# Kernel tuning notes

Measured on AMD Instinct MI355X. Metric: run time of the kernel, lower is better.

Reference implementation:

```python
import math
import jax, jax.numpy as jnp
import numpy as np

T, B, E, H = 1024, 4, 1024, 16
DH = E // H
NUM_BUCKETS = 32
MAX_DISTANCE = 128


def setup_inputs() -> dict:
    key = jax.random.key(0)
    ks = jax.random.split(key, 12)
    s = 0.02
    return {
        "query": jax.random.normal(ks[0], (T, B, E), dtype=jnp.float32),
        "q_w": jax.random.normal(ks[1], (E, E), dtype=jnp.float32) * s,
        "q_b": jax.random.normal(ks[2], (E,), dtype=jnp.float32) * s,
        "k_w": jax.random.normal(ks[3], (E, E), dtype=jnp.float32) * s,
        "k_b": jax.random.normal(ks[4], (E,), dtype=jnp.float32) * s,
        "v_w": jax.random.normal(ks[5], (E, E), dtype=jnp.float32) * s,
        "v_b": jax.random.normal(ks[6], (E,), dtype=jnp.float32) * s,
        "out_w": jax.random.normal(ks[7], (E, E), dtype=jnp.float32) * s,
        "out_b": jnp.zeros((E,), dtype=jnp.float32),
        "rel_bias": jax.random.normal(ks[8], (NUM_BUCKETS, H), dtype=jnp.float32) * s,
        "grep_w": jax.random.normal(ks[9], (8, DH), dtype=jnp.float32) * s,
        "grep_b": jax.random.normal(ks[10], (8,), dtype=jnp.float32) * s,
        "grep_a": jnp.ones((1, H, 1, 1), dtype=jnp.float32),
    }


def _relative_position_buckets(qlen, klen):
    # bidirectional T5-style bucketing
    ctx = jnp.arange(qlen, dtype=jnp.int32)[:, None]
    mem = jnp.arange(klen, dtype=jnp.int32)[None, :]
    rp = mem - ctx  # [qlen, klen]
    n = NUM_BUCKETS // 2
    buckets = (rp > 0).astype(jnp.int32) * n
    arp = jnp.abs(rp)
    max_exact = n // 2
    is_small = arp < max_exact
    # guard log(0): values at arp<max_exact are never selected from the large branch
    large = max_exact + (
        jnp.log(jnp.maximum(arp, 1).astype(jnp.float32) / max_exact)
        / math.log(MAX_DISTANCE / max_exact)
        * (n - max_exact)
    ).astype(jnp.int32)
    large = jnp.minimum(large, n - 1)
    return buckets + jnp.where(is_small, arp, large)


def reference(query, q_w, q_b, k_w, k_b, v_w, v_b, out_w, out_b, rel_bias, grep_w, grep_b, grep_a):
    tgt_len, bsz, embed_dim = query.shape
    scaling = DH ** -0.5

    # relative-position bias [H, T, T]
    buckets = _relative_position_buckets(tgt_len, tgt_len)
    pos_bias = rel_bias[buckets]                     # [T, T, H]
    pos_bias = jnp.transpose(pos_bias, (2, 0, 1))    # [H, T, T]

    # GRU-style gate computed from the *unprojected* query, per head
    qh_raw = jnp.transpose(query, (1, 0, 2)).reshape(bsz, tgt_len, H, DH)
    qh_raw = jnp.transpose(qh_raw, (0, 2, 1, 3))     # [B, H, T, DH]
    g = jnp.einsum("bhtd,ed->bhte", qh_raw, grep_w) + grep_b  # [B,H,T,8]
    g = jax.nn.sigmoid(g.reshape(bsz, H, tgt_len, 2, 4).sum(-1))  # [B,H,T,2]
    gate_a, gate_b = g[..., 0:1], g[..., 1:2]        # [B,H,T,1]
    gate_a_1 = gate_a * (gate_b * grep_a - 1.0) + 2.0
    attn_bias = gate_a_1 * pos_bias[None]            # [B, H, T, T]

    # QKV projections (self-attention: k,v from query)
    q = (query @ q_w.T + q_b) * scaling
    k = query @ k_w.T + k_b
    v = query @ v_w.T + v_b
    qh = jnp.transpose(q.reshape(tgt_len, bsz, H, DH), (1, 2, 0, 3))  # [B,H,T,DH]
    kh = jnp.transpose(k.reshape(tgt_len, bsz, H, DH), (1, 2, 0, 3))
    vh = jnp.transpose(v.reshape(tgt_len, bsz, H, DH), (1, 2, 0, 3))

    scores = jnp.einsum("bhtd,bhsd->bhts", qh, kh) + attn_bias
    probs = jax.nn.softmax(scores, axis=-1)
    ctx = jnp.einsum("bhts,bhsd->bhtd", probs, vh)   # [B,H,T,DH]
    ctx = jnp.transpose(ctx, (2, 0, 1, 3)).reshape(tgt_len, bsz, embed_dim)
    out = ctx @ out_w.T + out_b                      # [T, B, E]
    return out
```

## Files before the change

kernel.cpp:

```cpp
#include <hip/hip_runtime.h>
#include <math.h>

#define T_ 1024
#define B_ 4
#define E_ 1024
#define H_ 16
#define DH_ 64

#define LOG2E 1.44269504088896f

typedef __attribute__((ext_vector_type(8))) __bf16 bf16x8;
typedef __attribute__((ext_vector_type(4))) __bf16 bf16x4;
typedef __attribute__((ext_vector_type(4))) float f32x4;

__device__ __forceinline__ __bf16 f2bf(float x){
  union { unsigned short u; __bf16 b; } cv;
  unsigned u32 = __float_as_uint(x);
  cv.u = (unsigned short)((u32 + 0x7fffu + ((u32 >> 16) & 1u)) >> 16);
  return cv.b;
}
__device__ __forceinline__ __bf16 f2bf_fast(float x){
  union { unsigned short u; __bf16 b; } cv;
  cv.u = (unsigned short)((__float_as_uint(x) + 0x8000u) >> 16);
  return cv.b;
}

__device__ __forceinline__ void glds16(const void* g, void* l){
  __builtin_amdgcn_global_load_lds(
      (__attribute__((address_space(1))) void*)(void*)g,
      (__attribute__((address_space(3))) void*)l,
      16, 0, 0);
}

__global__ __launch_bounds__(256) void prep_kernel(
    const float* __restrict__ q_w, const float* __restrict__ k_w,
    const float* __restrict__ v_w, const float* __restrict__ out_w,
    __bf16* __restrict__ wq, __bf16* __restrict__ wk,
    __bf16* __restrict__ wv, __bf16* __restrict__ wo,
    const float* __restrict__ query, const float* __restrict__ gw,
    const float* __restrict__ gb, const float* __restrict__ ga,
    float* __restrict__ gates, __bf16* __restrict__ qbf,
    const float* __restrict__ rel_bias, float* __restrict__ tab)
{
  const int bid = blockIdx.x;
  const int tid = threadIdx.x;
  if (bid < 4096){
    const float* a; __bf16* o;
    switch (bid >> 10){
      case 0: a = q_w;  o = wq; break;
      case 1: a = k_w;  o = wk; break;
      case 2: a = v_w;  o = wv; break;
      default: a = out_w; o = wo; break;
    }
    int i = ((bid & 1023) * 256 + tid) * 4;
    float4 v = *(const float4*)(a + i);
    bf16x4 r;
    r[0] = f2bf(v.x); r[1] = f2bf(v.y); r[2] = f2bf(v.z); r[3] = f2bf(v.w);
    *(bf16x4*)(o + i) = r;
  } else if (bid < 4352){
    int t = (bid - 4096) * 4 + (tid >> 6);
    int bh = tid & 63;
    int h = bh & 15;
    const float* q = query + (size_t)t * E_ * B_ + bh * 64;
    __bf16* qo = qbf + (size_t)t * E_ * B_ + bh * 64;
    float g[8];
    #pragma unroll
    for (int e = 0; e < 8; e++) g[e] = gb[e];
    #pragma unroll
    for (int c = 0; c < 8; c++){
      float4 v0 = *(const float4*)(q + c * 8);
      float4 v1 = *(const float4*)(q + c * 8 + 4);
      bf16x8 o;
      o[0] = f2bf(v0.x); o[1] = f2bf(v0.y); o[2] = f2bf(v0.z); o[3] = f2bf(v0.w);
      o[4] = f2bf(v1.x); o[5] = f2bf(v1.y); o[6] = f2bf(v1.z); o[7] = f2bf(v1.w);
      *(bf16x8*)(qo + c * 8) = o;
      #pragma unroll
      for (int e = 0; e < 8; e++){
        const float* w = gw + e * 64 + c * 8;
        g[e] += v0.x * w[0] + v0.y * w[1] + v0.z * w[2] + v0.w * w[3]
              + v1.x * w[4] + v1.y * w[5] + v1.z * w[6] + v1.w * w[7];
      }
    }
    float a0 = (g[0] + g[1]) + (g[2] + g[3]);
    float a1 = (g[4] + g[5]) + (g[6] + g[7]);
    float sa = 1.f / (1.f + __expf(-a0));
    float sb = 1.f / (1.f + __expf(-a1));
    gates[bh * T_ + t] = (sa * (sb * ga[h] - 1.0f) + 2.0f) * LOG2E;
  } else {
    int tb = bid - 4352;
    int h = tb >> 3;
    int i = (tb & 7) * 256 + tid;
    if (i < 2047){
      int rp = i - 1023;
      int base = rp > 0 ? 16 : 0;
      int arp = rp < 0 ? -rp : rp;
      int off;
      if (arp < 8) off = arp;
      else {
        float val = (logf((float)arp * 0.125f) / 2.772588722239781f) * 8.0f;
        int lg = (int)val;
        off = 8 + (lg > 7 ? 7 : lg);
      }
      tab[h * 2047 + i] = rel_bias[(base + off) * H_ + h];
    }
  }
}

__global__ __launch_bounds__(256, 2) void gemm_qkv(
    const __bf16* __restrict__ A,
    const __bf16* __restrict__ W0, const __bf16* __restrict__ W1, const __bf16* __restrict__ W2,
    const float* __restrict__ b0, const float* __restrict__ b1, const float* __restrict__ b2,
    __bf16* out0, __bf16* out1, __bf16* out2)
{
  __shared__ __bf16 As[2][128 * 64];
  __shared__ __bf16 Bs[2][3][64 * 64];
  const int tid = threadIdx.x;
  const int lane = tid & 63, wid = tid >> 6;
  const int l15 = lane & 15, quad = lane >> 4;
  const int dd = blockIdx.x;
  const int j = dd >> 3;
  const int m0 = ((dd & 7) * 4 + (j & 3)) * 128;
  const int nt = j >> 2;
  const int n0 = nt * 64;

  f32x4 acc[3][2][4];
  #pragma unroll
  for (int z = 0; z < 3; z++)
    #pragma unroll
    for (int i = 0; i < 2; i++)
      #pragma unroll
      for (int jj = 0; jj < 4; jj++){
        acc[z][i][jj][0] = 0.f; acc[z][i][jj][1] = 0.f;
        acc[z][i][jj][2] = 0.f; acc[z][i][jj][3] = 0.f;
      }

  const int grow = lane >> 3;
  const int gcol = (((lane & 7) ^ grow) * 8);
  const int sw = (l15 & 7);

  auto STAGE = [&](int bi, int k0){
    #pragma unroll
    for (int r = 0; r < 4; r++){
      int rb = wid * 32 + r * 8;
      glds16(A + (size_t)(m0 + rb + grow) * E_ + k0 + gcol, &As[bi][rb * 64]);
    }
    #pragma unroll
    for (int r = 0; r < 2; r++){
      int rb = wid * 16 + r * 8;
      glds16(W0 + (size_t)(n0 + rb + grow) * E_ + k0 + gcol, &Bs[bi][0][rb * 64]);
      glds16(W1 + (size_t)(n0 + rb + grow) * E_ + k0 + gcol, &Bs[bi][1][rb * 64]);
      glds16(W2 + (size_t)(n0 + rb + grow) * E_ + k0 + gcol, &Bs[bi][2][rb * 64]);
    }
  };

  auto COMPUTE = [&](int bi){
    #pragma unroll
    for (int kq = 0; kq < 2; kq++){
      const int ce = ((kq * 4 + quad) ^ sw) * 8;
      bf16x8 am[2];
      #pragma unroll
      for (int i = 0; i < 2; i++) am[i] = *(const bf16x8*)&As[bi][(wid * 32 + i * 16 + l15) * 64 + ce];
      #pragma unroll
      for (int z = 0; z < 3; z++){
        bf16x8 bn[4];
        #pragma unroll
        for (int jj = 0; jj < 4; jj++) bn[jj] = *(const bf16x8*)&Bs[bi][z][(jj * 16 + l15) * 64 + ce];
        #pragma unroll
        for (int i = 0; i < 2; i++)
          #pragma unroll
          for (int jj = 0; jj < 4; jj++)
            acc[z][i][jj] = __builtin_amdgcn_mfma_f32_16x16x32_bf16(am[i], bn[jj], acc[z][i][jj], 0, 0, 0);
      }
    }
  };

  STAGE(0, 0);
  __syncthreads();
  for (int kt = 0; kt < 16; kt += 2){
    STAGE(1, (kt + 1) * 64);
    COMPUTE(0);
    __syncthreads();
    if (kt + 2 < 16) STAGE(0, (kt + 2) * 64);
    COMPUTE(1);
    __syncthreads();
  }

  #pragma unroll
  for (int z = 0; z < 2; z++){
    __bf16* outp = z ? out1 : out0;
    const float* bias = z ? b1 : b0;
    const float scale = z ? 1.0f : 0.125f * LOG2E;
    #pragma unroll
    for (int i = 0; i < 2; i++){
      const int row0 = m0 + wid * 32 + i * 16 + quad * 4;
      #pragma unroll
      for (int jj = 0; jj < 4; jj++){
        const int col = n0 + jj * 16 + l15;
        const float bc = bias[col];
        const int d2 = col & 63;
        #pragma unroll
        for (int r = 0; r < 4; r++){
          float v = (acc[z][i][jj][r] + bc) * scale;
          int row = row0 + r;
          int t = row >> 2, bb = row & 3;
          outp[(size_t)((bb * H_ + nt) * T_ + t) * DH_ + d2] = f2bf(v);
        }
      }
    }
  }

  __syncthreads();
  __bf16 (*vbuf)[4][32] = (__bf16 (*)[4][32])&As[0][0];
  #pragma unroll
  for (int i = 0; i < 2; i++){
    const int t_local = wid * 8 + i * 4 + quad;
    #pragma unroll
    for (int jj = 0; jj < 4; jj++){
      const int nl = jj * 16 + l15;
      const float bc = b2[n0 + nl];
      #pragma unroll
      for (int r = 0; r < 4; r++)
        vbuf[nl][r][t_local] = f2bf(acc[2][i][jj][r] + bc);
    }
  }
  __syncthreads();
  {
    const int nl = tid >> 2;
    const int bb = tid & 3;
    __bf16* dst = out2 + (size_t)((bb * H_ + nt) * DH_ + nl) * T_ + (m0 >> 2);
    const __bf16* src = &vbuf[nl][bb][0];
    #pragma unroll
    for (int c = 0; c < 4; c++)
      *(bf16x8*)(dst + c * 8) = *(const bf16x8*)(src + c * 8);
  }
}

__global__ __launch_bounds__(256) void gemm_out(
    const __bf16* __restrict__ A, const __bf16* __restrict__ W,
    const float* __restrict__ bias, float* __restrict__ out)
{
  __shared__ __bf16 As[2][64 * 64];
  __shared__ __bf16 Bs[2][128 * 64];
  const int tid = threadIdx.x;
  const int lane = tid & 63, wid = tid >> 6;
  const int l15 = lane & 15, quad = lane >> 4;
  const int wm = wid >> 1, wn = wid & 1;
  const int dd = blockIdx.x;
  const int j = dd >> 3;
  const int m0 = ((dd & 7) * 8 + (j & 7)) * 64;
  const int n0 = (j >> 3) * 128;

  f32x4 acc[2][4];
  #pragma unroll
  for (int i = 0; i < 2; i++)
    #pragma unroll
    for (int jj = 0; jj < 4; jj++){
      acc[i][jj][0] = 0.f; acc[i][jj][1] = 0.f; acc[i][jj][2] = 0.f; acc[i][jj][3] = 0.f;
    }

  const int grow = lane >> 3;
  const int gcol = (((lane & 7) ^ grow) * 8);
  const int sw = (l15 & 7);

  auto STAGE = [&](int bi, int k0){
    #pragma unroll
    for (int r = 0; r < 2; r++){
      int rbA = wid * 16 + r * 8;
      glds16(A + (size_t)(m0 + rbA + grow) * E_ + k0 + gcol, &As[bi][rbA * 64]);
    }
    #pragma unroll
    for (int r = 0; r < 4; r++){
      int rbB = wid * 32 + r * 8;
      glds16(W + (size_t)(n0 + rbB + grow) * E_ + k0 + gcol, &Bs[bi][rbB * 64]);
    }
  };

  auto COMPUTE = [&](int bi){
    #pragma unroll
    for (int kq = 0; kq < 2; kq++){
      const int ce = ((kq * 4 + quad) ^ sw) * 8;
      bf16x8 am[2], bn[4];
      #pragma unroll
      for (int i = 0; i < 2; i++) am[i] = *(const bf16x8*)&As[bi][(wm * 32 + i * 16 + l15) * 64 + ce];
      #pragma unroll
      for (int jj = 0; jj < 4; jj++) bn[jj] = *(const bf16x8*)&Bs[bi][(wn * 64 + jj * 16 + l15) * 64 + ce];
      #pragma unroll
      for (int i = 0; i < 2; i++)
        #pragma unroll
        for (int jj = 0; jj < 4; jj++)
          acc[i][jj] = __builtin_amdgcn_mfma_f32_16x16x32_bf16(am[i], bn[jj], acc[i][jj], 0, 0, 0);
    }
  };

  STAGE(0, 0);
  __syncthreads();
  for (int kt = 0; kt < 16; kt += 2){
    STAGE(1, (kt + 1) * 64);
    COMPUTE(0);
    __syncthreads();
    if (kt + 2 < 16) STAGE(0, (kt + 2) * 64);
    COMPUTE(1);
    __syncthreads();
  }

  #pragma unroll
  for (int i = 0; i < 2; i++){
    const int row0 = m0 + wm * 32 + i * 16 + quad * 4;
    #pragma unroll
    for (int jj = 0; jj < 4; jj++){
      const int col = n0 + wn * 64 + jj * 16 + l15;
      const float bc = bias[col];
      #pragma unroll
      for (int r = 0; r < 4; r++)
        out[(size_t)(row0 + r) * E_ + col] = acc[i][jj][r] + bc;
    }
  }
}

__global__ __launch_bounds__(256) void attn_kernel(
    const __bf16* __restrict__ qg, const __bf16* __restrict__ kg, const __bf16* __restrict__ vgT,
    const float* __restrict__ gates, const float* __restrict__ tab,
    __bf16* __restrict__ ctx)
{
  const int LDP = 72;
  __shared__ __bf16 Ks[2][64 * 64];
  __shared__ __bf16 Vt[2][64 * 64];
  __shared__ __bf16 Pt[4][2][16 * LDP];
  __shared__ float tabh[2048];

  const int tid = threadIdx.x;
  const int lane = tid & 63, wid = tid >> 6;
  const int l15 = lane & 15, quad = lane >> 4;
  const int dgrid = blockIdx.x;
  const int j = dgrid >> 3;
  const int bh = (dgrid & 7) + 8 * (j & 7);
  const int tq = j >> 3;
  const int b = bh >> 4, h = bh & 15;
  const __bf16* qb = qg + (size_t)bh * T_ * DH_;
  const __bf16* kb = kg + (size_t)bh * T_ * DH_;
  const __bf16* vb = vgT + (size_t)bh * DH_ * T_;

  for (int i = tid; i < 2047; i += 256) tabh[i] = tab[h * 2047 + i];

  const int t0w = tq * 128 + wid * 32;
  bf16x8 bq[2][2];
  float g[2];
  int ibase[2];
  #pragma unroll
  for (int tg = 0; tg < 2; tg++){
    int t_lane = t0w + tg * 16 + l15;
    bq[tg][0] = *(const bf16x8*)(qb + (size_t)t_lane * DH_ + quad * 8);
    bq[tg][1] = *(const bf16x8*)(qb + (size_t)t_lane * DH_ + 32 + quad * 8);
    g[tg] = gates[bh * T_ + t_lane];
    ibase[tg] = 1023 - t_lane;
  }

  const int grow = lane >> 3;
  const int gcol = (((lane & 7) ^ grow) * 8);
  const int swf = (l15 & 7);

  float l_run[2] = {0.f, 0.f};
  f32x4 O[2][4];
  #pragma unroll
  for (int tg = 0; tg < 2; tg++)
    #pragma unroll
    for (int mt = 0; mt < 4; mt++){ O[tg][mt][0]=0.f; O[tg][mt][1]=0.f; O[tg][mt][2]=0.f; O[tg][mt][3]=0.f; }

  #pragma unroll
  for (int r = 0; r < 2; r++){
    int rb = wid * 16 + r * 8;
    glds16(kb + (size_t)(rb + grow) * DH_ + gcol, &Ks[0][rb * 64]);
    glds16(vb + (size_t)(rb + grow) * T_ + gcol, &Vt[0][rb * 64]);
  }
  __syncthreads();

  for (int it = 0; it < 16; it++){
    const int s0 = it * 64;
    const int cur = it & 1;

    if (it < 15){
      const int sn = s0 + 64;
      #pragma unroll
      for (int r = 0; r < 2; r++){
        int rb = wid * 16 + r * 8;
        glds16(kb + (size_t)(sn + rb + grow) * DH_ + gcol, &Ks[cur ^ 1][rb * 64]);
        glds16(vb + (size_t)(rb + grow) * T_ + sn + gcol, &Vt[cur ^ 1][rb * 64]);
      }
    }

    f32x4 S[2][4];
    #pragma unroll
    for (int nt = 0; nt < 4; nt++){
      const int rowb = (nt * 16 + l15) * 64;
      bf16x8 ak0 = *(const bf16x8*)&Ks[cur][rowb + ((quad ^ swf) * 8)];
      bf16x8 ak1 = *(const bf16x8*)&Ks[cur][rowb + (((4 + quad) ^ swf) * 8)];
      #pragma unroll
      for (int tg = 0; tg < 2; tg++){
        f32x4 a; a[0]=0.f; a[1]=0.f; a[2]=0.f; a[3]=0.f;
        a = __builtin_amdgcn_mfma_f32_16x16x32_bf16(ak0, bq[tg][0], a, 0, 0, 0);
        a = __builtin_amdgcn_mfma_f32_16x16x32_bf16(ak1, bq[tg][1], a, 0, 0, 0);
        S[tg][nt] = a;
      }
    }

    const int drel = s0 - t0w;
    if (drel >= 160 || drel <= -192){
      const float sv = (drel > 0) ? tabh[1151] : tabh[895];
      #pragma unroll
      for (int tg = 0; tg < 2; tg++){
        const float cb = g[tg] * sv;
        #pragma unroll
        for (int nt = 0; nt < 4; nt++)
          #pragma unroll
          for (int r = 0; r < 4; r++)
            S[tg][nt][r] = __builtin_amdgcn_exp2f(S[tg][nt][r] + cb);
      }
    } else {
      #pragma unroll
      for (int tg = 0; tg < 2; tg++){
        const int ib = ibase[tg] + s0;
        #pragma unroll
        for (int nt = 0; nt < 4; nt++)
          #pragma unroll
          for (int r = 0; r < 4; r++)
            S[tg][nt][r] = __builtin_amdgcn_exp2f(S[tg][nt][r] + g[tg] * tabh[ib + nt * 16 + quad * 4 + r]);
      }
    }

    #pragma unroll
    for (int tg = 0; tg < 2; tg++){
      __bf16* pw = &Pt[wid][tg][0];
      #pragma unroll
      for (int nt = 0; nt < 4; nt++){
        bf16x4 p;
        p[0] = f2bf_fast(S[tg][nt][0]); p[1] = f2bf_fast(S[tg][nt][1]);
        p[2] = f2bf_fast(S[tg][nt][2]); p[3] = f2bf_fast(S[tg][nt][3]);
        *(bf16x4*)&pw[l15 * LDP + nt * 16 + quad * 4] = p;
      }
      float rs = 0.f;
      #pragma unroll
      for (int nt = 0; nt < 4; nt++) rs += (S[tg][nt][0] + S[tg][nt][1]) + (S[tg][nt][2] + S[tg][nt][3]);
      rs += __shfl_xor(rs, 16, 64);
      rs += __shfl_xor(rs, 32, 64);
      l_run[tg] += rs;
    }

    #pragma unroll
    for (int ks = 0; ks < 2; ks++){
      bf16x8 bp[2];
      #pragma unroll
      for (int tg = 0; tg < 2; tg++)
        bp[tg] = *(const bf16x8*)&Pt[wid][tg][l15 * LDP + ks * 32 + quad * 8];
      #pragma unroll
      for (int mt = 0; mt < 4; mt++){
        const int rowb = (mt * 16 + l15) * 64;
        bf16x8 av = *(const bf16x8*)&Vt[cur][rowb + (((ks * 4 + quad) ^ swf) * 8)];
        #pragma unroll
        for (int tg = 0; tg < 2; tg++)
          O[tg][mt] = __builtin_amdgcn_mfma_f32_16x16x32_bf16(av, bp[tg], O[tg][mt], 0, 0, 0);
      }
    }

    __syncthreads();
  }

  #pragma unroll
  for (int tg = 0; tg < 2; tg++){
    const int t_lane = t0w + tg * 16 + l15;
    const float inv = 1.f / l_run[tg];
    #pragma unroll
    for (int mt = 0; mt < 4; mt++){
      bf16x4 o;
      o[0] = f2bf(O[tg][mt][0] * inv); o[1] = f2bf(O[tg][mt][1] * inv);
      o[2] = f2bf(O[tg][mt][2] * inv); o[3] = f2bf(O[tg][mt][3] * inv);
      *(bf16x4*)&ctx[(size_t)(t_lane * B_ + b) * E_ + h * DH_ + mt * 16 + quad * 4] = o;
    }
  }
}

extern "C" void kernel_launch(void* const* d_in, const int* in_sizes, int n_in,
                              void* d_out, int out_size, void* d_ws, size_t ws_size,
                              hipStream_t stream)
{
  (void)in_sizes; (void)n_in; (void)out_size; (void)ws_size;
  const float* query    = (const float*)d_in[0];
  const float* q_w      = (const float*)d_in[1];
  const float* q_b      = (const float*)d_in[2];
  const float* k_w      = (const float*)d_in[3];
  const float* k_b      = (const float*)d_in[4];
  const float* v_w      = (const float*)d_in[5];
  const float* v_b      = (const float*)d_in[6];
  const float* out_w    = (const float*)d_in[7];
  const float* out_b    = (const float*)d_in[8];
  const float* rel_bias = (const float*)d_in[9];
  const float* grep_w   = (const float*)d_in[10];
  const float* grep_b   = (const float*)d_in[11];
  const float* grep_a   = (const float*)d_in[12];

  char* ws = (char*)d_ws;
  size_t off = 0;
  __bf16* qbf = (__bf16*)(ws + off); off += (size_t)4096 * 1024 * 2;
  __bf16* wq  = (__bf16*)(ws + off); off += (size_t)1024 * 1024 * 2;
  __bf16* wk  = (__bf16*)(ws + off); off += (size_t)1024 * 1024 * 2;
  __bf16* wv  = (__bf16*)(ws + off); off += (size_t)1024 * 1024 * 2;
  __bf16* wo  = (__bf16*)(ws + off); off += (size_t)1024 * 1024 * 2;
  __bf16* qh  = (__bf16*)(ws + off); off += (size_t)4096 * 1024 * 2;
  __bf16* kh  = (__bf16*)(ws + off); off += (size_t)4096 * 1024 * 2;
  __bf16* vhT = (__bf16*)(ws + off); off += (size_t)4096 * 1024 * 2;
  __bf16* ctx = (__bf16*)(ws + off); off += (size_t)4096 * 1024 * 2;
  float* gates = (float*)(ws + off); off += (size_t)65536 * 4;
  float* tab   = (float*)(ws + off); off += (size_t)16 * 2047 * 4;

  prep_kernel<<<4480, 256, 0, stream>>>(q_w, k_w, v_w, out_w, wq, wk, wv, wo,
                                        query, grep_w, grep_b, grep_a, gates, qbf,
                                        rel_bias, tab);
  gemm_qkv<<<512, 256, 0, stream>>>(qbf, wq, wk, wv, q_b, k_b, v_b, qh, kh, vhT);
  attn_kernel<<<512, 256, 0, stream>>>(qh, kh, vhT, gates, tab, ctx);
  gemm_out<<<512, 256, 0, stream>>>(ctx, wo, out_b, (float*)d_out);
}
```

Baseline: 203.4 us.

## Enlarge QKV GEMM M-tile to 256 and single-buffer output GEMM

The fused QKV GEMM now gives each block a 256-row M tile, so 256 blocks are launched instead of 512 and each loaded weight tile is reused across more rows. The per-wave accumulator grows to 48 MFMA tiles and launch bounds drop to one block per CU to leave room for the extra registers, and the V transpose staging buffer is widened to match. Separately, the output GEMM drops its LDS double-buffering for a simple load, sync, compute loop, which lowers LDS use but removes the overlap between loads and compute. The larger tile cuts redundant weight traffic but leaves only 256 blocks on a chip with many CUs, which risks lower occupancy and poorer latency hiding.

```diff
diff --git a/kernel.cpp b/kernel.cpp
--- a/kernel.cpp
+++ b/kernel.cpp
@@ -106,28 +106,29 @@
   }
 }
 
-__global__ __launch_bounds__(256, 2) void gemm_qkv(
+__global__ __launch_bounds__(256, 1) void gemm_qkv(
     const __bf16* __restrict__ A,
     const __bf16* __restrict__ W0, const __bf16* __restrict__ W1, const __bf16* __restrict__ W2,
     const float* __restrict__ b0, const float* __restrict__ b1, const float* __restrict__ b2,
     __bf16* out0, __bf16* out1, __bf16* out2)
 {
-  __shared__ __bf16 As[2][128 * 64];
+  __shared__ __bf16 As[2][256 * 64];
   __shared__ __bf16 Bs[2][3][64 * 64];
   const int tid = threadIdx.x;
   const int lane = tid & 63, wid = tid >> 6;
   const int l15 = lane & 15, quad = lane >> 4;
   const int dd = blockIdx.x;
   const int j = dd >> 3;
-  const int m0 = ((dd & 7) * 4 + (j & 3)) * 128;
-  const int nt = j >> 2;
+  const int mi = (dd & 7) * 2 + (j & 1);
+  const int m0 = mi * 256;
+  const int nt = j >> 1;
   const int n0 = nt * 64;
 
-  f32x4 acc[3][2][4];
+  f32x4 acc[3][4][4];
   #pragma unroll
   for (int z = 0; z < 3; z++)
     #pragma unroll
-    for (int i = 0; i < 2; i++)
+    for (int i = 0; i < 4; i++)
       #pragma unroll
       for (int jj = 0; jj < 4; jj++){
         acc[z][i][jj][0] = 0.f; acc[z][i][jj][1] = 0.f;
@@ -140,8 +141,8 @@
 
   auto STAGE = [&](int bi, int k0){
     #pragma unroll
-    for (int r = 0; r < 4; r++){
-      int rb = wid * 32 + r * 8;
+    for (int r = 0; r < 8; r++){
+      int rb = wid * 64 + r * 8;
       glds16(A + (size_t)(m0 + rb + grow) * E_ + k0 + gcol, &As[bi][rb * 64]);
     }
     #pragma unroll
@@ -157,16 +158,16 @@
     #pragma unroll
     for (int kq = 0; kq < 2; kq++){
       const int ce = ((kq * 4 + quad) ^ sw) * 8;
-      bf16x8 am[2];
-      #pragma unroll
-      for (int i = 0; i < 2; i++) am[i] = *(const bf16x8*)&As[bi][(wid * 32 + i * 16 + l15) * 64 + ce];
+      bf16x8 am[4];
+      #pragma unroll
+      for (int i = 0; i < 4; i++) am[i] = *(const bf16x8*)&As[bi][(wid * 64 + i * 16 + l15) * 64 + ce];
       #pragma unroll
       for (int z = 0; z < 3; z++){
         bf16x8 bn[4];
         #pragma unroll
         for (int jj = 0; jj < 4; jj++) bn[jj] = *(const bf16x8*)&Bs[bi][z][(jj * 16 + l15) * 64 + ce];
         #pragma unroll
-        for (int i = 0; i < 2; i++)
+        for (int i = 0; i < 4; i++)
           #pragma unroll
           for (int jj = 0; jj < 4; jj++)
             acc[z][i][jj] = __builtin_amdgcn_mfma_f32_16x16x32_bf16(am[i], bn[jj], acc[z][i][jj], 0, 0, 0);
@@ -191,8 +192,8 @@
     const float* bias = z ? b1 : b0;
     const float scale = z ? 1.0f : 0.125f * LOG2E;
     #pragma unroll
-    for (int i = 0; i < 2; i++){
-      const int row0 = m0 + wid * 32 + i * 16 + quad * 4;
+    for (int i = 0; i < 4; i++){
+      const int row0 = m0 + wid * 64 + i * 16 + quad * 4;
       #pragma unroll
       for (int jj = 0; jj < 4; jj++){
         const int col = n0 + jj * 16 + l15;
@@ -210,17 +211,18 @@
   }
 
   __syncthreads();
-  __bf16 (*vbuf)[4][32] = (__bf16 (*)[4][32])&As[0][0];
-  #pragma unroll
-  for (int i = 0; i < 2; i++){
-    const int t_local = wid * 8 + i * 4 + quad;
+  __bf16 (*vbuf)[4][64] = (__bf16 (*)[4][64])&As[0][0];
+  #pragma unroll
+  for (int i = 0; i < 4; i++){
     #pragma unroll
     for (int jj = 0; jj < 4; jj++){
       const int nl = jj * 16 + l15;
       const float bc = b2[n0 + nl];
       #pragma unroll
-      for (int r = 0; r < 4; r++)
-        vbuf[nl][r][t_local] = f2bf(acc[2][i][jj][r] + bc);
+      for (int r = 0; r < 4; r++){
+        const int lr = wid * 64 + i * 16 + quad * 4 + r;
+        vbuf[nl][lr & 3][lr >> 2] = f2bf(acc[2][i][jj][r] + bc);
+      }
     }
   }
   __syncthreads();
@@ -230,7 +232,7 @@
     __bf16* dst = out2 + (size_t)((bb * H_ + nt) * DH_ + nl) * T_ + (m0 >> 2);
     const __bf16* src = &vbuf[nl][bb][0];
     #pragma unroll
-    for (int c = 0; c < 4; c++)
+    for (int c = 0; c < 8; c++)
       *(bf16x8*)(dst + c * 8) = *(const bf16x8*)(src + c * 8);
   }
 }
@@ -239,8 +241,8 @@
     const __bf16* __restrict__ A, const __bf16* __restrict__ W,
     const float* __restrict__ bias, float* __restrict__ out)
 {
-  __shared__ __bf16 As[2][64 * 64];
-  __shared__ __bf16 Bs[2][128 * 64];
+  __shared__ __bf16 As[64 * 64];
+  __shared__ __bf16 Bs[128 * 64];
   const int tid = threadIdx.x;
   const int lane = tid & 63, wid = tid >> 6;
   const int l15 = lane & 15, quad = lane >> 4;
@@ -262,45 +264,33 @@
   const int gcol = (((lane & 7) ^ grow) * 8);
   const int sw = (l15 & 7);
 
-  auto STAGE = [&](int bi, int k0){
+  for (int k0 = 0; k0 < E_; k0 += 64){
+    __syncthreads();
     #pragma unroll
     for (int r = 0; r < 2; r++){
       int rbA = wid * 16 + r * 8;
-      glds16(A + (size_t)(m0 + rbA + grow) * E_ + k0 + gcol, &As[bi][rbA * 64]);
+      glds16(A + (size_t)(m0 + rbA + grow) * E_ + k0 + gcol, &As[rbA * 64]);
     }
     #pragma unroll
     for (int r = 0; r < 4; r++){
       int rbB = wid * 32 + r * 8;
-      glds16(W + (size_t)(n0 + rbB + grow) * E_ + k0 + gcol, &Bs[bi][rbB * 64]);
-    }
-  };
-
-  auto COMPUTE = [&](int bi){
+      glds16(W + (size_t)(n0 + rbB + grow) * E_ + k0 + gcol, &Bs[rbB * 64]);
+    }
+    __syncthreads();
     #pragma unroll
     for (int kq = 0; kq < 2; kq++){
       const int ce = ((kq * 4 + quad) ^ sw) * 8;
       bf16x8 am[2], bn[4];
       #pragma unroll
-      for (int i = 0; i < 2; i++) am[i] = *(const bf16x8*)&As[bi][(wm * 32 + i * 16 + l15) * 64 + ce];
-      #pragma unroll
-      for (int jj = 0; jj < 4; jj++) bn[jj] = *(const bf16x8*)&Bs[bi][(wn * 64 + jj * 16 + l15) * 64 + ce];
+      for (int i = 0; i < 2; i++) am[i] = *(const bf16x8*)&As[(wm * 32 + i * 16 + l15) * 64 + ce];
+      #pragma unroll
+      for (int jj = 0; jj < 4; jj++) bn[jj] = *(const bf16x8*)&Bs[(wn * 64 + jj * 16 + l15) * 64 + ce];
       #pragma unroll
       for (int i = 0; i < 2; i++)
         #pragma unroll
         for (int jj = 0; jj < 4; jj++)
           acc[i][jj] = __builtin_amdgcn_mfma_f32_16x16x32_bf16(am[i], bn[jj], acc[i][jj], 0, 0, 0);
     }
-  };
-
-  STAGE(0, 0);
-  __syncthreads();
-  for (int kt = 0; kt < 16; kt += 2){
-    STAGE(1, (kt + 1) * 64);
-    COMPUTE(0);
-    __syncthreads();
-    if (kt + 2 < 16) STAGE(0, (kt + 2) * 64);
-    COMPUTE(1);
-    __syncthreads();
   }
 
   #pragma unroll
@@ -514,7 +504,7 @@
   prep_kernel<<<4480, 256, 0, stream>>>(q_w, k_w, v_w, out_w, wq, wk, wv, wo,
                                         query, grep_w, grep_b, grep_a, gates, qbf,
                                         rel_bias, tab);
-  gemm_qkv<<<512, 256, 0, stream>>>(qbf, wq, wk, wv, q_b, k_b, v_b, qh, kh, vhT);
+  gemm_qkv<<<256, 256, 0, stream>>>(qbf, wq, wk, wv, q_b, k_b, v_b, qh, kh, vhT);
   attn_kernel<<<512, 256, 0, stream>>>(qh, kh, vhT, gates, tab, ctx);
   gemm_out<<<512, 256, 0, stream>>>(ctx, wo, out_b, (float*)d_out);
 }
```

After: 206.4 us. About the same (+1.5%).
